# Performance work log

Hardware: AMD Instinct MI355X
Metric: run time of the kernel (lower is better)

Reference implementation:

```python
import jax, jax.numpy as jnp
import numpy as np

D_MODEL = 1024
N_HEADS = 16
N_GROUPS = 4
HEAD_DIM = D_MODEL // N_HEADS          # 64
HPG = N_HEADS // N_GROUPS              # heads per group = 4
KV_DIM = N_GROUPS * HEAD_DIM           # 256


def setup_inputs() -> dict:
    key = jax.random.key(0)
    ks = jax.random.split(key, 9)
    B, T = 2, 2048
    s = 0.02
    return {
        "x":  jax.random.normal(ks[0], (B, T, D_MODEL), dtype=jnp.float32),
        "Wq": jax.random.normal(ks[1], (D_MODEL, D_MODEL), dtype=jnp.float32) * s,
        "bq": jnp.zeros((D_MODEL,), dtype=jnp.float32),
        "Wk": jax.random.normal(ks[2], (D_MODEL, KV_DIM), dtype=jnp.float32) * s,
        "bk": jnp.zeros((KV_DIM,), dtype=jnp.float32),
        "Wv": jax.random.normal(ks[3], (D_MODEL, KV_DIM), dtype=jnp.float32) * s,
        "bv": jnp.zeros((KV_DIM,), dtype=jnp.float32),
        "Wo": jax.random.normal(ks[4], (D_MODEL, D_MODEL), dtype=jnp.float32) * s,
        "bo": jnp.zeros((D_MODEL,), dtype=jnp.float32),
    }


def reference(x, Wq, bq, Wk, bk, Wv, bv, Wo, bo):
    B, T, C = x.shape
    q = x @ Wq + bq                                   # [B,T,C]
    k = x @ Wk + bk                                   # [B,T,G*hd]
    v = x @ Wv + bv

    # [B, G, hpg, T, hd] for q; [B, G, T, hd] for k,v (native GQA head sharing,
    # equivalent to repeat_interleave on the group dim in the torch code)
    q = q.reshape(B, T, N_GROUPS, HPG, HEAD_DIM).transpose(0, 2, 3, 1, 4)
    k = k.reshape(B, T, N_GROUPS, HEAD_DIM).transpose(0, 2, 1, 3)
    v = v.reshape(B, T, N_GROUPS, HEAD_DIM).transpose(0, 2, 1, 3)

    scale = 1.0 / jnp.sqrt(jnp.float32(HEAD_DIM))
    attn = jnp.einsum('bghqd,bgkd->bghqk', q, k) * scale   # [B,G,hpg,T,T]

    causal = jnp.tril(jnp.ones((T, T), dtype=bool))        # True = keep
    attn = jnp.where(causal, attn, jnp.float32(-jnp.inf))
    attn = jax.nn.softmax(attn, axis=-1)
    # dropout p=0.1 only in training mode; reference is eval mode (identity)

    out = jnp.einsum('bghqk,bgkd->bghqd', attn, v)         # [B,G,hpg,T,hd]
    out = out.transpose(0, 3, 1, 2, 4).reshape(B, T, C)
    return out @ Wo + bo
```

## Files before the change

kernel.cpp:

```cpp
#include <hip/hip_runtime.h>
#include <hip/hip_bf16.h>
#include <stdint.h>

#define D_MODEL 1024
#define T_LEN   2048
#define BATCH   2
#define N_HEADS 16
#define KV_DIM  256
#define QKV_N   1536
#define M_ROWS  (BATCH * T_LEN)

typedef unsigned short u16;
typedef __bf16 bf16x8 __attribute__((ext_vector_type(8)));
typedef __bf16 bf16x2 __attribute__((ext_vector_type(2)));
typedef float  f32x4  __attribute__((ext_vector_type(4)));
typedef uint32_t u32x4v __attribute__((ext_vector_type(4)));

__device__ __forceinline__ u16 f2b(float f) {
    uint32_t u = __builtin_bit_cast(uint32_t, f);
    u += 0x7FFFu + ((u >> 16) & 1u);
    return (u16)(u >> 16);
}

__device__ __forceinline__ uint32_t pk_bf16(float a, float b) {
#if __has_builtin(__builtin_amdgcn_cvt_pk_bf16_f32)
    bf16x2 v = __builtin_amdgcn_cvt_pk_bf16_f32(a, b);
    return __builtin_bit_cast(uint32_t, v);
#else
    return (uint32_t)f2b(a) | ((uint32_t)f2b(b) << 16);
#endif
}

__device__ __forceinline__ void gl_lds16(const void* g, void* l) {
    __builtin_amdgcn_global_load_lds(g, l, 16, 0, 0);
}

__constant__ unsigned char LPT_TBL[48] = {
    62, 63, 60, 15, 61, 58, 59, 56,
    50, 53, 13, 52, 55, 54, 57, 14,
    51, 48, 12, 49, 46, 47, 44, 11,
    39, 38, 41, 10, 40, 43, 42, 45,
    36,  9, 37, 34, 35, 32,  8, 33,
     0,  1,  2,  3,  4,  5,  6,  7
};

__global__ __launch_bounds__(256) void prep(
    const float* __restrict__ x,
    const float* __restrict__ Wq, const float* __restrict__ Wk,
    const float* __restrict__ Wv, const float* __restrict__ Wo,
    u16* __restrict__ xb, u16* __restrict__ WcatT, u16* __restrict__ WoT)
{
    __shared__ u16 tile[32][33];
    int id = blockIdx.x;
    int tid = threadIdx.x;
    if (id < 2048) {
        int i = (id * 256 + tid) * 8;
        float4 a = *(const float4*)&x[i];
        float4 c = *(const float4*)&x[i + 4];
        u16 r[8] = { f2b(a.x), f2b(a.y), f2b(a.z), f2b(a.w),
                     f2b(c.x), f2b(c.y), f2b(c.z), f2b(c.w) };
        *(uint4*)&xb[i] = *(const uint4*)r;
        return;
    }
    int t = id - 2048;
    int bx = t % 80;
    int k0 = (t / 80) * 32;
    const float* src; u16* dst; int N, n0;
    if (bx < 32)       { src = Wq; dst = WcatT;                   N = 1024; n0 = bx * 32; }
    else if (bx < 40)  { src = Wk; dst = WcatT + 1024 * 1024;     N = 256;  n0 = (bx - 32) * 32; }
    else if (bx < 48)  { src = Wv; dst = WcatT + 1280 * 1024;     N = 256;  n0 = (bx - 40) * 32; }
    else               { src = Wo; dst = WoT;                     N = 1024; n0 = (bx - 48) * 32; }
    for (int i = 0; i < 4; ++i) {
        int idx = tid + i * 256;
        int r = idx >> 5, c = idx & 31;
        tile[r][c] = f2b(src[(size_t)(k0 + r) * N + (n0 + c)]);
    }
    __syncthreads();
    for (int i = 0; i < 4; ++i) {
        int idx = tid + i * 256;
        int r = idx >> 5, c = idx & 31;
        dst[(size_t)(n0 + r) * 1024 + (k0 + c)] = tile[c][r];
    }
}

__global__ __launch_bounds__(256) void gemm_qkv(
    const u16* __restrict__ A, const u16* __restrict__ BT,
    const float* __restrict__ bq, const float* __restrict__ bk,
    const float* __restrict__ bv, u16* __restrict__ Qb,
    u16* __restrict__ Kpack, u16* __restrict__ Vpack)
{
    constexpr int K = 1024;
    constexpr float SCALE = 0.125f * 1.44269504088896f;
    __shared__ __align__(16) u16 As[64 * 64];
    __shared__ __align__(16) u16 Bs[128 * 64];

    int tid  = threadIdx.x;
    int lane = tid & 63, w = tid >> 6;
    int quad = lane >> 4, l15 = lane & 15;
    int m0 = blockIdx.y * 64, n0 = blockIdx.x * 128;
    int lr = lane >> 3, lc = (lane & 7) * 8;

    f32x4 acc[4][2] = {};

    for (int k0 = 0; k0 < K; k0 += 64) {
        for (int t = 0; t < 2; ++t) {
            int rb = t * 32 + w * 8;
            gl_lds16(&A[(size_t)(m0 + rb + lr) * K + k0 + lc], &As[rb * 64]);
        }
        for (int t = 0; t < 4; ++t) {
            int rb = t * 32 + w * 8;
            gl_lds16(&BT[(size_t)(n0 + rb + lr) * K + k0 + lc], &Bs[rb * 64]);
        }
        __syncthreads();
        for (int kk = 0; kk < 64; kk += 32) {
            bf16x8 a[4], b[2];
            for (int i = 0; i < 4; ++i)
                a[i] = *(const bf16x8*)&As[(i * 16 + l15) * 64 + kk + quad * 8];
            for (int j = 0; j < 2; ++j)
                b[j] = *(const bf16x8*)&Bs[(w * 32 + j * 16 + l15) * 64 + kk + quad * 8];
            for (int i = 0; i < 4; ++i)
                for (int j = 0; j < 2; ++j)
                    acc[i][j] = __builtin_amdgcn_mfma_f32_16x16x32_bf16(
                        a[i], b[j], acc[i][j], 0, 0, 0);
        }
        __syncthreads();
    }

    for (int j = 0; j < 2; ++j) {
        int col = n0 + w * 32 + j * 16 + l15;
        float bj = (col < 1024) ? bq[col] : (col < 1280) ? bk[col - 1024] : bv[col - 1280];
        for (int i = 0; i < 4; ++i) {
            int rowb = m0 + i * 16 + quad * 4;
            int bb = rowb >> 11, keyloc = rowb & 2047;
            int t64 = keyloc >> 6;
            if (col < 1024) {
                for (int r = 0; r < 4; ++r)
                    Qb[(size_t)(rowb + r) * 1024 + col] =
                        f2b((acc[i][j][r] + bj) * SCALE);
            } else if (col < 1280) {
                int d = col - 1024; int g = d >> 6; d &= 63;
                int kk = d >> 5, qd = (d >> 3) & 3, e = d & 7;
                int ntk = (keyloc >> 4) & 3, l15k = keyloc & 15;
                size_t base = ((((size_t)(bb * 4 + g) * 32 + t64) * 2 + kk) * 4
                               + ntk) * 512 + qd * 128 + l15k * 8 + e;
                for (int r = 0; r < 4; ++r)
                    Kpack[base + r * 8] = f2b(acc[i][j][r] + bj);
            } else {
                int d = col - 1280; int g = d >> 6; d &= 63;
                int dt = d >> 4, l15v = d & 15;
                int kkp = (keyloc >> 5) & 1, qv = (keyloc >> 3) & 3, e0 = keyloc & 7;
                u16 tmp[4];
                for (int r = 0; r < 4; ++r) tmp[r] = f2b(acc[i][j][r] + bj);
                size_t base = ((((size_t)(bb * 4 + g) * 32 + t64) * 2 + kkp) * 4
                               + dt) * 512 + (qv * 16 + l15v) * 8 + e0;
                *(uint64_t*)&Vpack[base] = *(const uint64_t*)tmp;
            }
        }
    }
}

__global__ __launch_bounds__(256) void gemm_out(
    const u16* __restrict__ A, const u16* __restrict__ BT,
    const float* __restrict__ bias, float* __restrict__ C)
{
    constexpr int K = 1024, N = 1024;
    __shared__ __align__(16) u16 As[64 * 64];
    __shared__ __align__(16) u16 Bs[128 * 64];

    int tid  = threadIdx.x;
    int lane = tid & 63, w = tid >> 6;
    int quad = lane >> 4, l15 = lane & 15;
    int m0 = blockIdx.y * 64, n0 = blockIdx.x * 128;
    int lr = lane >> 3, lc = (lane & 7) * 8;

    f32x4 acc[4][2] = {};

    for (int k0 = 0; k0 < K; k0 += 64) {
        for (int t = 0; t < 2; ++t) {
            int rb = t * 32 + w * 8;
            gl_lds16(&A[(size_t)(m0 + rb + lr) * K + k0 + lc], &As[rb * 64]);
        }
        for (int t = 0; t < 4; ++t) {
            int rb = t * 32 + w * 8;
            gl_lds16(&BT[(size_t)(n0 + rb + lr) * K + k0 + lc], &Bs[rb * 64]);
        }
        __syncthreads();
        for (int kk = 0; kk < 64; kk += 32) {
            bf16x8 a[4], b[2];
            for (int i = 0; i < 4; ++i)
                a[i] = *(const bf16x8*)&As[(i * 16 + l15) * 64 + kk + quad * 8];
            for (int j = 0; j < 2; ++j)
                b[j] = *(const bf16x8*)&Bs[(w * 32 + j * 16 + l15) * 64 + kk + quad * 8];
            for (int i = 0; i < 4; ++i)
                for (int j = 0; j < 2; ++j)
                    acc[i][j] = __builtin_amdgcn_mfma_f32_16x16x32_bf16(
                        a[i], b[j], acc[i][j], 0, 0, 0);
        }
        __syncthreads();
    }

    for (int j = 0; j < 2; ++j) {
        int col = n0 + w * 32 + j * 16 + l15;
        float bj = bias[col];
        for (int i = 0; i < 4; ++i) {
            int rowb = m0 + i * 16 + quad * 4;
            for (int r = 0; r < 4; ++r)
                C[(size_t)(rowb + r) * N + col] = acc[i][j][r] + bj;
        }
    }
}

__global__ __launch_bounds__(256, 6) void attn_kernel(
    const u16* __restrict__ Qb,
    const u16* __restrict__ Kpack,
    const u16* __restrict__ Vpack,
    u16* __restrict__ AO,
    float* __restrict__ Opart,
    float* __restrict__ Lpart)
{
    constexpr int LDP = 72;
    __shared__ __align__(16) u16 Kv[4096];
    __shared__ __align__(16) u16 Vv[4096];
    __shared__ __align__(16) u16 Ps[4][16 * LDP];

    int tid  = threadIdx.x;
    int lane = tid & 63, w = tid >> 6;
    int quad = lane >> 4, l15 = lane & 15;

    int gid = blockIdx.x;
    int bg = gid & 7;
    int b = bg >> 2, g = bg & 3;
    int idx = gid >> 3;
    int code = LPT_TBL[idx >> 2];
    int kq = idx & 3;
    int q4, h = 0, tgB, tgE;
    bool split;
    if (code < 32) {
        split = false; q4 = code; tgB = 0; tgE = q4 + 1;
    } else {
        split = true; q4 = code >> 1; h = code & 1;
        int nA = (q4 + 2) >> 1;
        tgB = h ? nA : 0;
        tgE = h ? (q4 + 1) : nA;
    }
    int j = q4 * 4 + kq;
    int head = g * 4 + w;
    int q0 = j * 16;
    int iters64 = q4 + 1;

    const u16* Qp = Qb + ((size_t)b * T_LEN + q0) * 1024 + head * 64;
    const u16* Kp = Kpack + (size_t)bg * 131072;
    const u16* Vp = Vpack + (size_t)bg * 131072;
    u16*       Op = AO + ((size_t)b * T_LEN + q0) * D_MODEL + head * 64;
    u16* Pw = Ps[w];

    bf16x8 Qfrag[2];
    #pragma unroll
    for (int kk = 0; kk < 2; ++kk)
        Qfrag[kk] = *(const bf16x8*)&Qp[(size_t)l15 * 1024 + kk * 32 + quad * 8];

    u32x4v onesbits = {0x3F803F80u, 0x3F803F80u, 0x3F803F80u, 0x3F803F80u};
    bf16x8 vones = __builtin_bit_cast(bf16x8, onesbits);

    f32x4 o[4] = {};
    f32x4 o_l = {};
    int qrow = q0 + l15;

    for (int tg = tgB; tg < tgE; ++tg) {
        bool diag = (tg == iters64 - 1);

        const u16* kt = Kp + (size_t)tg * 4096;
        const u16* vt = Vp + (size_t)tg * 4096;
        #pragma unroll
        for (int c = 0; c < 2; ++c) {
            int ch = w * 2 + c;
            gl_lds16(kt + ch * 512 + lane * 8, &Kv[ch * 512]);
            gl_lds16(vt + ch * 512 + lane * 8, &Vv[ch * 512]);
        }
        __syncthreads();

        f32x4 sacc[4] = {};
        #pragma unroll
        for (int kk = 0; kk < 2; ++kk) {
            bf16x8 bQ = Qfrag[kk];
            #pragma unroll
            for (int ntk = 0; ntk < 4; ++ntk) {
                bf16x8 aK = *(const bf16x8*)&Kv[(kk * 4 + ntk) * 512 + lane * 8];
                sacc[ntk] = __builtin_amdgcn_mfma_f32_16x16x32_bf16(
                    aK, bQ, sacc[ntk], 0, 0, 0);
            }
        }
        #pragma unroll
        for (int ntk = 0; ntk < 4; ++ntk) {
            float p0, p1, p2, p3;
            if (diag) {
                int key = tg * 64 + ntk * 16 + quad * 4;
                p0 = (key + 0 <= qrow) ? exp2f(sacc[ntk][0]) : 0.f;
                p1 = (key + 1 <= qrow) ? exp2f(sacc[ntk][1]) : 0.f;
                p2 = (key + 2 <= qrow) ? exp2f(sacc[ntk][2]) : 0.f;
                p3 = (key + 3 <= qrow) ? exp2f(sacc[ntk][3]) : 0.f;
            } else {
                p0 = exp2f(sacc[ntk][0]);
                p1 = exp2f(sacc[ntk][1]);
                p2 = exp2f(sacc[ntk][2]);
                p3 = exp2f(sacc[ntk][3]);
            }
            uint2 pv;
            pv.x = pk_bf16(p0, p1);
            pv.y = pk_bf16(p2, p3);
            *(uint2*)&Pw[l15 * LDP + ntk * 16 + quad * 4] = pv;
        }

        #pragma unroll
        for (int kkp = 0; kkp < 2; ++kkp) {
            bf16x8 aP = *(const bf16x8*)&Pw[l15 * LDP + kkp * 32 + quad * 8];
            #pragma unroll
            for (int dt = 0; dt < 4; ++dt) {
                bf16x8 bV = *(const bf16x8*)&Vv[(kkp * 4 + dt) * 512 + lane * 8];
                o[dt] = __builtin_amdgcn_mfma_f32_16x16x32_bf16(
                    aP, bV, o[dt], 0, 0, 0);
            }
            o_l = __builtin_amdgcn_mfma_f32_16x16x32_bf16(
                aP, vones, o_l, 0, 0, 0);
        }
        __syncthreads();
    }

    if (!split) {
        float li[4];
        #pragma unroll
        for (int r = 0; r < 4; ++r)
            li[r] = 1.0f / o_l[r];
        #pragma unroll
        for (int dt = 0; dt < 4; ++dt)
            #pragma unroll
            for (int r = 0; r < 4; ++r)
                Op[(size_t)(quad * 4 + r) * D_MODEL + dt * 16 + l15] =
                    f2b(o[dt][r] * li[r]);
    } else {
        int p = ((bg * 16 + (q4 - 16)) * 4 + kq) * 2 + h;
        size_t obase = (size_t)(p * 4 + w) * 1024;
        #pragma unroll
        for (int dt = 0; dt < 4; ++dt)
            #pragma unroll
            for (int r = 0; r < 4; ++r)
                Opart[obase + (size_t)(quad * 4 + r) * 64 + dt * 16 + l15] =
                    o[dt][r];
        if (l15 == 0) {
            #pragma unroll
            for (int r = 0; r < 4; ++r)
                Lpart[(size_t)(p * 4 + w) * 16 + quad * 4 + r] = o_l[r];
        }
    }
}

__global__ __launch_bounds__(64) void attn_combine(
    const float* __restrict__ Opart, const float* __restrict__ Lpart,
    u16* __restrict__ AO)
{
    int gid = blockIdx.x;
    int w  = gid & 3;
    int sp = gid >> 2;
    int bg = sp >> 6;
    int rest = sp & 63;
    int q4 = 16 + (rest >> 2);
    int kq = rest & 3;
    int b = bg >> 2, g = bg & 3;
    int head = g * 4 + w;
    int j = q4 * 4 + kq;
    int q0 = j * 16;
    int pA = ((bg * 16 + (q4 - 16)) * 4 + kq) * 2;

    const float* OA = Opart + (size_t)(pA * 4 + w) * 1024;
    const float* OB = Opart + (size_t)((pA + 1) * 4 + w) * 1024;
    const float* LA = Lpart + (size_t)(pA * 4 + w) * 16;
    const float* LB = Lpart + (size_t)((pA + 1) * 4 + w) * 16;

    int d = threadIdx.x;
    #pragma unroll 4
    for (int row = 0; row < 16; ++row) {
        float l = LA[row] + LB[row];
        float linv = 1.0f / l;
        float v = OA[row * 64 + d] + OB[row * 64 + d];
        AO[((size_t)(b * T_LEN + q0 + row)) * D_MODEL + head * 64 + d] =
            f2b(v * linv);
    }
}

extern "C" void kernel_launch(void* const* d_in, const int* in_sizes, int n_in,
                              void* d_out, int out_size, void* d_ws, size_t ws_size,
                              hipStream_t stream) {
    const float* x  = (const float*)d_in[0];
    const float* Wq = (const float*)d_in[1];
    const float* bq = (const float*)d_in[2];
    const float* Wk = (const float*)d_in[3];
    const float* bk = (const float*)d_in[4];
    const float* Wv = (const float*)d_in[5];
    const float* bv = (const float*)d_in[6];
    const float* Wo = (const float*)d_in[7];
    const float* bo = (const float*)d_in[8];
    float* out = (float*)d_out;

    u16* ws    = (u16*)d_ws;
    u16* xb    = ws;  ws += (size_t)M_ROWS * 1024;
    u16* WcatT = ws;  ws += (size_t)QKV_N * 1024;
    u16* WoT   = ws;  ws += 1024 * 1024;
    u16* Qb    = ws;  ws += (size_t)M_ROWS * 1024;
    u16* Kpack = ws;  ws += (size_t)M_ROWS * KV_DIM;
    u16* Vpack = ws;  ws += (size_t)M_ROWS * KV_DIM;
    float* Opart = (float*)ws;
    float* Lpart = Opart + (size_t)1024 * 4 * 1024;
    u16* AO    = xb;

    prep<<<2048 + 2560, 256, 0, stream>>>(x, Wq, Wk, Wv, Wo, xb, WcatT, WoT);
    gemm_qkv<<<dim3(QKV_N / 128, M_ROWS / 64), 256, 0, stream>>>(
        xb, WcatT, bq, bk, bv, Qb, Kpack, Vpack);
    attn_kernel<<<1536, 256, 0, stream>>>(Qb, Kpack, Vpack, AO, Opart, Lpart);
    attn_combine<<<2048, 64, 0, stream>>>(Opart, Lpart, AO);
    gemm_out<<<dim3(1024 / 128, M_ROWS / 64), 256, 0, stream>>>(AO, WoT, bo, out);
}
```

Baseline: 173.7 us.

## Fuse split-KV combine into attention kernel via atomic ticket flags

Removes the separate attn_combine launch. Each split attention block now writes its partial output, fences, and takes an atomic ticket on a per-pair flag. The block that arrives second adds in its partner's partial O and L, then writes the normalized bf16 output directly. Flags are zeroed by an extra block in the prep kernel. This saves a kernel launch and a pass over the partials, at the cost of atomics, fences and a serialized tail for the second arriver.

Result: slower. 386.8 us (+122.7%).

```diff
diff --git a/kernel.cpp b/kernel.cpp
--- a/kernel.cpp
+++ b/kernel.cpp
@@ -48,11 +48,17 @@
     const float* __restrict__ x,
     const float* __restrict__ Wq, const float* __restrict__ Wk,
     const float* __restrict__ Wv, const float* __restrict__ Wo,
-    u16* __restrict__ xb, u16* __restrict__ WcatT, u16* __restrict__ WoT)
+    u16* __restrict__ xb, u16* __restrict__ WcatT, u16* __restrict__ WoT,
+    unsigned int* __restrict__ flags)
 {
     __shared__ u16 tile[32][33];
     int id = blockIdx.x;
     int tid = threadIdx.x;
+    if (id == 4608) {
+        flags[tid] = 0u;
+        flags[tid + 256] = 0u;
+        return;
+    }
     if (id < 2048) {
         int i = (id * 256 + tid) * 8;
         float4 a = *(const float4*)&x[i];
@@ -216,12 +222,14 @@
     const u16* __restrict__ Vpack,
     u16* __restrict__ AO,
     float* __restrict__ Opart,
-    float* __restrict__ Lpart)
+    float* __restrict__ Lpart,
+    unsigned int* __restrict__ flags)
 {
     constexpr int LDP = 72;
     __shared__ __align__(16) u16 Kv[4096];
     __shared__ __align__(16) u16 Vv[4096];
     __shared__ __align__(16) u16 Ps[4][16 * LDP];
+    __shared__ unsigned int ticket;
 
     int tid  = threadIdx.x;
     int lane = tid & 63, w = tid >> 6;
@@ -338,7 +346,8 @@
                 Op[(size_t)(quad * 4 + r) * D_MODEL + dt * 16 + l15] =
                     f2b(o[dt][r] * li[r]);
     } else {
-        int p = ((bg * 16 + (q4 - 16)) * 4 + kq) * 2 + h;
+        int pbase = ((bg * 16 + (q4 - 16)) * 4 + kq) * 2;
+        int p = pbase + h;
         size_t obase = (size_t)(p * 4 + w) * 1024;
         #pragma unroll
         for (int dt = 0; dt < 4; ++dt)
@@ -351,39 +360,33 @@
             for (int r = 0; r < 4; ++r)
                 Lpart[(size_t)(p * 4 + w) * 16 + quad * 4 + r] = o_l[r];
         }
-    }
-}
-
-__global__ __launch_bounds__(64) void attn_combine(
-    const float* __restrict__ Opart, const float* __restrict__ Lpart,
-    u16* __restrict__ AO)
-{
-    int gid = blockIdx.x;
-    int w  = gid & 3;
-    int sp = gid >> 2;
-    int bg = sp >> 6;
-    int rest = sp & 63;
-    int q4 = 16 + (rest >> 2);
-    int kq = rest & 3;
-    int b = bg >> 2, g = bg & 3;
-    int head = g * 4 + w;
-    int j = q4 * 4 + kq;
-    int q0 = j * 16;
-    int pA = ((bg * 16 + (q4 - 16)) * 4 + kq) * 2;
-
-    const float* OA = Opart + (size_t)(pA * 4 + w) * 1024;
-    const float* OB = Opart + (size_t)((pA + 1) * 4 + w) * 1024;
-    const float* LA = Lpart + (size_t)(pA * 4 + w) * 16;
-    const float* LB = Lpart + (size_t)((pA + 1) * 4 + w) * 16;
-
-    int d = threadIdx.x;
-    #pragma unroll 4
-    for (int row = 0; row < 16; ++row) {
-        float l = LA[row] + LB[row];
-        float linv = 1.0f / l;
-        float v = OA[row * 64 + d] + OB[row * 64 + d];
-        AO[((size_t)(b * T_LEN + q0 + row)) * D_MODEL + head * 64 + d] =
-            f2b(v * linv);
+        __threadfence();
+        __syncthreads();
+        if (tid == 0)
+            ticket = atomicAdd(&flags[pbase >> 1], 1u);
+        __syncthreads();
+        if (ticket == 1u) {
+            __threadfence();
+            int po = pbase + (1 - h);
+            size_t ob2 = (size_t)(po * 4 + w) * 1024;
+            #pragma unroll
+            for (int dt = 0; dt < 4; ++dt)
+                #pragma unroll
+                for (int r = 0; r < 4; ++r)
+                    o[dt][r] += Opart[ob2 + (size_t)(quad * 4 + r) * 64
+                                      + dt * 16 + l15];
+            float li[4];
+            #pragma unroll
+            for (int r = 0; r < 4; ++r)
+                li[r] = 1.0f / (o_l[r] +
+                        Lpart[(size_t)(po * 4 + w) * 16 + quad * 4 + r]);
+            #pragma unroll
+            for (int dt = 0; dt < 4; ++dt)
+                #pragma unroll
+                for (int r = 0; r < 4; ++r)
+                    Op[(size_t)(quad * 4 + r) * D_MODEL + dt * 16 + l15] =
+                        f2b(o[dt][r] * li[r]);
+        }
     }
 }
 
@@ -410,12 +413,14 @@
     u16* Vpack = ws;  ws += (size_t)M_ROWS * KV_DIM;
     float* Opart = (float*)ws;
     float* Lpart = Opart + (size_t)1024 * 4 * 1024;
+    unsigned int* flags = (unsigned int*)(Lpart + (size_t)1024 * 4 * 16);
     u16* AO    = xb;
 
-    prep<<<2048 + 2560, 256, 0, stream>>>(x, Wq, Wk, Wv, Wo, xb, WcatT, WoT);
+    prep<<<2048 + 2560 + 1, 256, 0, stream>>>(x, Wq, Wk, Wv, Wo, xb, WcatT, WoT,
+                                              flags);
     gemm_qkv<<<dim3(QKV_N / 128, M_ROWS / 64), 256, 0, stream>>>(
         xb, WcatT, bq, bk, bv, Qb, Kpack, Vpack);
-    attn_kernel<<<1536, 256, 0, stream>>>(Qb, Kpack, Vpack, AO, Opart, Lpart);
-    attn_combine<<<2048, 64, 0, stream>>>(Opart, Lpart, AO);
+    attn_kernel<<<1536, 256, 0, stream>>>(Qb, Kpack, Vpack, AO, Opart, Lpart,
+                                          flags);
     gemm_out<<<dim3(1024 / 128, M_ROWS / 64), 256, 0, stream>>>(AO, WoT, bo, out);
 }
```
